# Performance work log

Hardware: AMD Instinct MI355X
Metric: run time of the kernel (lower is better)

## Reference

```python
import jax, jax.numpy as jnp
import numpy as np

EMBED = 768
DIM = 800          # embed + 32 gender features
IN_C = 1024
GRID = 32          # img_size // patch_size(=1)
LN_EPS = 1e-5      # torch nn.LayerNorm default


def setup_inputs() -> dict:
    key = jax.random.key(0)
    ks = jax.random.split(key, 8)
    B = 32
    x = jax.random.normal(ks[0], (B, IN_C, GRID, GRID), dtype=jnp.float32)
    gender_encode = jax.random.normal(ks[1], (B, 32), dtype=jnp.float32)
    # PatchEmbed 1x1 conv (acts as per-pixel linear) + LayerNorm params
    conv_w = jax.random.normal(ks[2], (EMBED, IN_C), dtype=jnp.float32) * (IN_C ** -0.5)
    conv_b = jnp.zeros((EMBED,), dtype=jnp.float32)
    ln_g = jnp.ones((EMBED,), dtype=jnp.float32)
    ln_b = jnp.zeros((EMBED,), dtype=jnp.float32)
    cls_token = jax.random.normal(ks[3], (1, 1, EMBED), dtype=jnp.float32) * 0.02
    # Attention qkv linear (bias=True); proj is never used in the forward path
    qkv_w = jax.random.normal(ks[4], (3 * DIM, DIM), dtype=jnp.float32) * (DIM ** -0.5)
    qkv_b = jnp.zeros((3 * DIM,), dtype=jnp.float32)
    return {
        "x": x, "gender_encode": gender_encode,
        "conv_w": conv_w, "conv_b": conv_b,
        "ln_g": ln_g, "ln_b": ln_b,
        "cls_token": cls_token,
        "qkv_w": qkv_w, "qkv_b": qkv_b,
    }


def _forward(x, gender_encode, conv_w, conv_b, ln_g, ln_b, cls_token, qkv_w, qkv_b):
    B = x.shape[0]
    # PatchEmbed: 1x1 conv stride 1 == per-pixel linear; flatten(2).transpose(1,2)
    p = jnp.einsum('bchw,oc->bhwo', x, conv_w) + conv_b        # [B,32,32,768]
    p = p.reshape(B, GRID * GRID, EMBED)                        # [B,1024,768]
    mu = jnp.mean(p, axis=-1, keepdims=True)
    var = jnp.mean((p - mu) ** 2, axis=-1, keepdims=True)
    p = (p - mu) * jax.lax.rsqrt(var + LN_EPS) * ln_g + ln_b
    # prepend cls token, concat broadcast gender features
    cls = jnp.broadcast_to(cls_token, (B, 1, EMBED))
    t = jnp.concatenate([cls, p], axis=1)                       # [B,1025,768]
    g = jnp.broadcast_to(gender_encode[:, None, :], (B, t.shape[1], 32))
    t = jnp.concatenate([t, g], axis=2)                         # [B,1025,800]
    # Attention (note: self.norm / proj / v are unused in the original forward)
    qkv = t @ qkv_w.T + qkv_b                                   # [B,1025,2400]
    q = qkv[..., 0:DIM]
    k = qkv[..., DIM:2 * DIM]
    scale = DIM ** -0.5
    # only the cls-query row is ever used -> compute just that row
    scores = jnp.einsum('bc,bnc->bn', q[:, 0], k) * scale       # [B,1025]
    attn_cls = jax.nn.softmax(scores[:, 1:], axis=-1)           # [B,1024]
    return attn_cls.reshape(B, 1, GRID, GRID)


def reference(x, gender_encode, conv_w, conv_b, ln_g, ln_b, cls_token, qkv_w, qkv_b):
    return _forward(x, gender_encode, conv_w, conv_b, ln_g, ln_b, cls_token, qkv_w, qkv_b)
```

## Files before the change

kernel.cpp:

```cpp
#include <hip/hip_runtime.h>
#include <hip/hip_bf16.h>

#define EMBED 768
#define DIMQ  800
#define INC   1024
#define NPIX  1024

typedef __bf16 bf16_t;
typedef __bf16 bf16x8 __attribute__((ext_vector_type(8)));
typedef __bf16 bf16x2 __attribute__((ext_vector_type(2)));
typedef float  f32x4  __attribute__((ext_vector_type(4)));

#define GLD_LDS(gp, lp) __builtin_amdgcn_global_load_lds( \
    (const __attribute__((address_space(1))) void*)(gp),  \
    (__attribute__((address_space(3))) void*)(lp), 16, 0, 0)

__global__ __launch_bounds__(256)
void k_prep(const float* __restrict__ x, bf16_t* __restrict__ xT,
            const float* __restrict__ w, bf16_t* __restrict__ cw,
            const float* __restrict__ qkv_w, const float* __restrict__ qkv_b,
            const float* __restrict__ cls, const float* __restrict__ gender,
            float* __restrict__ q0b) {
    __shared__ __align__(16) unsigned int tile[64 * 36];
    const int bi = blockIdx.x;
    const int t  = threadIdx.x;
    if (bi < 8192) {
        const int b  = bi >> 8;
        const int k0 = ((bi >> 4) & 15) * 64;
        const int m0 = (bi & 15) * 64;
        const int m_l = t & 63;
        const int wv  = t >> 6;
        const float* src = x + ((size_t)(b * 1024 + k0 + wv * 16) * 1024) + m0 + m_l;
        bf16x2* trow = (bf16x2*)tile;
#pragma unroll
        for (int i = 0; i < 8; ++i) {
            float a0 = src[(size_t)(2 * i) * 1024];
            float a1 = src[(size_t)(2 * i + 1) * 1024];
            bf16x2 p; p[0] = (bf16_t)a0; p[1] = (bf16_t)a1;
            trow[m_l * 36 + wv * 8 + i] = p;
        }
        __syncthreads();
        const int m_r = t >> 2;
        bf16_t* drow = xT + ((size_t)(b * 1024 + m0 + m_r) * 1024) + k0;
#pragma unroll
        for (int rep = 0; rep < 2; ++rep) {
            int j = (t & 3) + rep * 4;
            bf16x8 v = *(const bf16x8*)&tile[m_r * 36 + j * 4];
            int slot = j ^ (m_r & 7);
            *(bf16x8*)(drow + slot * 8) = v;
        }
    } else if (bi < 8392) {
        const int wv = t >> 6, tl = t & 63;
        const int i = (bi - 8192) * 4 + wv;
        const float* row = qkv_w + (size_t)i * DIMQ;
        float ps = 0.f;
        for (int j = tl; j < EMBED; j += 64) ps += row[j] * cls[j];
#pragma unroll
        for (int off = 1; off < 64; off <<= 1) ps += __shfl_xor(ps, off, 64);
        if (tl < 32) {
            float g = 0.f;
#pragma unroll
            for (int j = 0; j < 32; ++j) g += row[EMBED + j] * gender[tl * 32 + j];
            q0b[tl * DIMQ + i] = ps + g + qkv_b[i];
        }
    } else {
        const int i = (bi - 8392) * 256 + t;
        const int n = i >> 10, k = i & 1023;
        const int s = (k >> 3) & 7;
        const int src_k = (k & ~63) | (((s ^ (n & 7)) & 7) << 3) | (k & 7);
        cw[i] = (bf16_t)w[(size_t)n * 1024 + src_k];
    }
}

__global__ __launch_bounds__(256)
void k_u(const float* __restrict__ qkv_w, const float* __restrict__ q0b,
         const float* __restrict__ ln_g, float* __restrict__ u) {
    __shared__ float q0s[DIMQ];
    __shared__ float sh[8][33];
    int t = threadIdx.x;
    int b  = blockIdx.x / 24;
    int j0 = (blockIdx.x % 24) * 32;
    for (int i = t; i < DIMQ; i += 256) q0s[i] = q0b[b * DIMQ + i];
    __syncthreads();
    int j_l = t & 31, os = t >> 5;
    const float* wk = qkv_w + (size_t)DIMQ * DIMQ;
    const float* wp = wk + (size_t)(os * 100) * DIMQ + j0 + j_l;
    float acc = 0.f;
#pragma unroll 4
    for (int i = 0; i < 100; ++i) acc += wp[(size_t)i * DIMQ] * q0s[os * 100 + i];
    sh[os][j_l] = acc;
    __syncthreads();
    if (t < 32) {
        float s = 0.f;
#pragma unroll
        for (int o = 0; o < 8; ++o) s += sh[o][t];
        u[b * EMBED + j0 + t] = s * ln_g[j0 + t];
    }
}

__global__ __launch_bounds__(512, 2)
void k_main(const bf16_t* __restrict__ xT, const bf16_t* __restrict__ cw,
            const float* __restrict__ conv_b, const float* __restrict__ u,
            float* __restrict__ partial) {
    extern __shared__ unsigned char smem[];

    const int tid = threadIdx.x;
    const int bi = blockIdx.x;
    const int x8 = bi & 7;
    const int s  = bi >> 3;
    const int nt = s % 3;
    const int mt = (s / 3) * 8 + x8;
    const int b  = mt >> 2;
    const int gm = mt * 256;
    const int gn = nt * 256;

    const int wv = tid >> 6;
    const int l  = tid & 63;
    const int lr = l >> 3;
    const int lc = l & 7;

    const int col  = l & 15;
    const int quad = l >> 4;
    const int wm   = (wv >> 2) * 128;
    const int wn   = (wv & 3) * 64;

    bf16_t* A0 = (bf16_t*)(smem);
    bf16_t* B0 = (bf16_t*)(smem + 32768);
    bf16_t* A1 = (bf16_t*)(smem + 65536);
    bf16_t* B1 = (bf16_t*)(smem + 98304);

    const bf16_t* asrc = xT + (size_t)(gm + lr) * 1024 + lc * 8;
    const bf16_t* bsrc = cw + (size_t)(gn + lr) * 1024 + lc * 8;

    f32x4 C[8][4] = {};

#define ISSUE(tt, Ab, Bb) do {                                              \
        const size_t ko_ = (size_t)(tt) * 64;                               \
        _Pragma("unroll")                                                   \
        for (int j = 0; j < 4; ++j) {                                       \
            const int rg = j * 64 + wv * 8;                                 \
            GLD_LDS(asrc + (size_t)rg * 1024 + ko_, (Ab) + rg * 64);        \
            GLD_LDS(bsrc + (size_t)rg * 1024 + ko_, (Bb) + rg * 64);        \
        }                                                                   \
    } while (0)

    ISSUE(0, A0, B0);
    ISSUE(1, A1, B1);
    asm volatile("s_waitcnt vmcnt(8)" ::: "memory");
    asm volatile("s_barrier" ::: "memory");

    for (int t = 0; t < 16; ++t) {
        bf16_t* Ab = (t & 1) ? A1 : A0;
        bf16_t* Bb = (t & 1) ? B1 : B0;
#pragma unroll
        for (int ks = 0; ks < 2; ++ks) {
            bf16x8 bg[4];
#pragma unroll
            for (int ni = 0; ni < 4; ++ni) {
                const int r  = wn + ni * 16 + col;
                const int ph = (ks * 4 + quad) ^ (r & 7);
                bg[ni] = *(const bf16x8*)(Bb + r * 64 + ph * 8);
            }
#pragma unroll
            for (int g = 0; g < 2; ++g) {
                bf16x8 af[4];
#pragma unroll
                for (int mi = 0; mi < 4; ++mi) {
                    const int r  = wm + (g * 4 + mi) * 16 + col;
                    const int ph = (ks * 4 + quad) ^ (r & 7);
                    af[mi] = *(const bf16x8*)(Ab + r * 64 + ph * 8);
                }
                __builtin_amdgcn_s_barrier();
                __builtin_amdgcn_s_setprio(1);
#pragma unroll
                for (int mi = 0; mi < 4; ++mi)
#pragma unroll
                    for (int ni = 0; ni < 4; ++ni)
                        C[g * 4 + mi][ni] = __builtin_amdgcn_mfma_f32_16x16x32_bf16(
                            af[mi], bg[ni], C[g * 4 + mi][ni], 0, 0, 0);
                __builtin_amdgcn_s_setprio(0);
                __builtin_amdgcn_s_barrier();
            }
        }
        if (t < 15) {
            asm volatile("s_barrier" ::: "memory");
            if (t + 2 < 16) {
                bf16_t* An = (t & 1) ? A1 : A0;
                bf16_t* Bn = (t & 1) ? B1 : B0;
                ISSUE(t + 2, An, Bn);
                asm volatile("s_waitcnt vmcnt(8)" ::: "memory");
            } else {
                asm volatile("s_waitcnt vmcnt(0)" ::: "memory");
            }
            asm volatile("s_barrier" ::: "memory");
        }
    }
#undef ISSUE

    float cb[4], uv[4];
#pragma unroll
    for (int ni = 0; ni < 4; ++ni) {
        const int og = gn + wn + ni * 16 + col;
        cb[ni] = conv_b[og];
        uv[ni] = u[b * EMBED + og];
    }
    float* part = (float*)smem;
    asm volatile("s_barrier" ::: "memory");
#pragma unroll
    for (int mi = 0; mi < 8; ++mi)
#pragma unroll
        for (int r = 0; r < 4; ++r) {
            float a = 0.f, sq = 0.f, d = 0.f;
#pragma unroll
            for (int ni = 0; ni < 4; ++ni) {
                float v = C[mi][ni][r] + cb[ni];
                a += v; sq += v * v; d += v * uv[ni];
            }
#pragma unroll
            for (int off = 1; off < 16; off <<= 1) {
                a  += __shfl_xor(a, off, 64);
                sq += __shfl_xor(sq, off, 64);
                d  += __shfl_xor(d, off, 64);
            }
            if (col == 0) {
                const int row = wm + mi * 16 + quad * 4 + r;
                float* pp = part + ((wv & 3) * 256 + row) * 3;
                pp[0] = a; pp[1] = sq; pp[2] = d;
            }
        }
    __syncthreads();
    if (tid < 256) {
        float s1 = 0.f, s2 = 0.f, s3 = 0.f;
#pragma unroll
        for (int g2 = 0; g2 < 4; ++g2) {
            const float* pp = part + (g2 * 256 + tid) * 3;
            s1 += pp[0]; s2 += pp[1]; s3 += pp[2];
        }
        const size_t pix = (size_t)gm + tid;
        partial[(size_t)(0 * 3 + nt) * 32768 + pix] = s1;
        partial[(size_t)(1 * 3 + nt) * 32768 + pix] = s2;
        partial[(size_t)(2 * 3 + nt) * 32768 + pix] = s3;
    }
}

__global__ __launch_bounds__(1024)
void k_final(const float* __restrict__ partial, const float* __restrict__ u,
             float* __restrict__ out) {
    __shared__ float red[16];
    __shared__ float bc[3];
    const int b = blockIdx.x, t = threadIdx.x;
    const int lane = t & 63, wid = t >> 6;

    float pu = (t < EMBED) ? u[b * EMBED + t] : 0.f;
#pragma unroll
    for (int off = 1; off < 64; off <<= 1) pu += __shfl_xor(pu, off, 64);
    if (lane == 0) red[wid] = pu;
    __syncthreads();
    if (t == 0) { float s = 0.f; for (int i = 0; i < 16; ++i) s += red[i]; bc[0] = s; }
    __syncthreads();
    const float Su = bc[0];

    const size_t m = (size_t)b * 1024 + t;
    float S1 = 0.f, S2 = 0.f, S3 = 0.f;
#pragma unroll
    for (int nt = 0; nt < 3; ++nt) {
        S1 += partial[(size_t)(0 * 3 + nt) * 32768 + m];
        S2 += partial[(size_t)(1 * 3 + nt) * 32768 + m];
        S3 += partial[(size_t)(2 * 3 + nt) * 32768 + m];
    }
    const float mu  = S1 * (1.f / 768.f);
    const float var = S2 * (1.f / 768.f) - mu * mu;
    const float sc  = 0.035355339059327376f * (S3 - mu * Su) * rsqrtf(var + 1e-5f);

    float mx = sc;
#pragma unroll
    for (int off = 1; off < 64; off <<= 1) mx = fmaxf(mx, __shfl_xor(mx, off, 64));
    if (lane == 0) red[wid] = mx;
    __syncthreads();
    if (t == 0) { float mm = -1e30f; for (int i = 0; i < 16; ++i) mm = fmaxf(mm, red[i]); bc[1] = mm; }
    __syncthreads();
    const float e = __expf(sc - bc[1]);
    float ss = e;
#pragma unroll
    for (int off = 1; off < 64; off <<= 1) ss += __shfl_xor(ss, off, 64);
    __syncthreads();
    if (lane == 0) red[wid] = ss;
    __syncthreads();
    if (t == 0) { float s = 0.f; for (int i = 0; i < 16; ++i) s += red[i]; bc[2] = s; }
    __syncthreads();
    out[m] = e / bc[2];
}

extern "C" void kernel_launch(void* const* d_in, const int* in_sizes, int n_in,
                              void* d_out, int out_size, void* d_ws, size_t ws_size,
                              hipStream_t stream) {
    const float* x      = (const float*)d_in[0];
    const float* gender = (const float*)d_in[1];
    const float* conv_w = (const float*)d_in[2];
    const float* conv_b = (const float*)d_in[3];
    const float* ln_g   = (const float*)d_in[4];
    const float* cls    = (const float*)d_in[6];
    const float* qkv_w  = (const float*)d_in[7];
    const float* qkv_b  = (const float*)d_in[8];
    float* out = (float*)d_out;

    char* ws = (char*)d_ws;
    bf16_t* cw      = (bf16_t*)ws;
    float*  q0b     = (float*)(ws + 1572864);
    float*  u       = (float*)(ws + 1675264);
    float*  partial = (float*)(ws + 1773568);
    bf16_t* xT      = (bf16_t*)(ws + 4132864);

    static bool s_attr = false;
    if (!s_attr) {
        hipFuncSetAttribute(reinterpret_cast<const void*>(k_main),
                            hipFuncAttributeMaxDynamicSharedMemorySize, 131072);
        s_attr = true;
    }

    hipLaunchKernelGGL(k_prep,  dim3(11464), dim3(256),  0, stream,
                       x, xT, conv_w, cw, qkv_w, qkv_b, cls, gender, q0b);
    hipLaunchKernelGGL(k_u,     dim3(768),   dim3(256),  0, stream, qkv_w, q0b, ln_g, u);
    hipLaunchKernelGGL(k_main,  dim3(384),   dim3(512),  131072, stream, xT, cw, conv_b, u, partial);
    hipLaunchKernelGGL(k_final, dim3(32),    dim3(1024), 0, stream, partial, u, out);
}
```

Measured before the change: 322.4 us.

## Stream conv weights from global into registers and retile N to 192

The conv weight (B operand) is no longer staged in LDS. Each wave now loads its B fragments straight from global memory into registers, one k-step ahead, so the weight swizzle in the prep kernel is dropped. The N tile shrinks from 256 to 192, which gives 512 blocks instead of 384 and four partial slices per pixel instead of three. The A tile moves to a triple-buffered LDS ring using 96KB, with a simpler barrier and wait scheme. In exchange, B traffic goes through L2 directly with less reuse, and the implicit waits on the register loads may also serialize the A prefetch.

```diff
diff --git a/kernel.cpp b/kernel.cpp
--- a/kernel.cpp
+++ b/kernel.cpp
@@ -65,10 +65,7 @@
         }
     } else {
         const int i = (bi - 8392) * 256 + t;
-        const int n = i >> 10, k = i & 1023;
-        const int s = (k >> 3) & 7;
-        const int src_k = (k & ~63) | (((s ^ (n & 7)) & 7) << 3) | (k & 7);
-        cw[i] = (bf16_t)w[(size_t)n * 1024 + src_k];
+        cw[i] = (bf16_t)w[i];
     }
 }
 
@@ -108,11 +105,11 @@
     const int bi = blockIdx.x;
     const int x8 = bi & 7;
     const int s  = bi >> 3;
-    const int nt = s % 3;
-    const int mt = (s / 3) * 8 + x8;
+    const int nt = s & 3;
+    const int mt = (s >> 2) * 8 + x8;
     const int b  = mt >> 2;
     const int gm = mt * 256;
-    const int gn = nt * 256;
+    const int gn = nt * 192;
 
     const int wv = tid >> 6;
     const int l  = tid & 63;
@@ -122,45 +119,55 @@
     const int col  = l & 15;
     const int quad = l >> 4;
     const int wm   = (wv >> 2) * 128;
-    const int wn   = (wv & 3) * 64;
-
-    bf16_t* A0 = (bf16_t*)(smem);
-    bf16_t* B0 = (bf16_t*)(smem + 32768);
-    bf16_t* A1 = (bf16_t*)(smem + 65536);
-    bf16_t* B1 = (bf16_t*)(smem + 98304);
+    const int wn   = (wv & 3) * 48;
 
     const bf16_t* asrc = xT + (size_t)(gm + lr) * 1024 + lc * 8;
-    const bf16_t* bsrc = cw + (size_t)(gn + lr) * 1024 + lc * 8;
-
-    f32x4 C[8][4] = {};
-
-#define ISSUE(tt, Ab, Bb) do {                                              \
+    const bf16_t* bgp  = cw + (size_t)(gn + wn + col) * 1024 + quad * 8;
+
+    f32x4 C[8][3] = {};
+    bf16x8 bgC[2][3], bgN[2][3];
+
+#define ISSUE_A(tt, dst) do {                                               \
         const size_t ko_ = (size_t)(tt) * 64;                               \
         _Pragma("unroll")                                                   \
         for (int j = 0; j < 4; ++j) {                                       \
             const int rg = j * 64 + wv * 8;                                 \
-            GLD_LDS(asrc + (size_t)rg * 1024 + ko_, (Ab) + rg * 64);        \
-            GLD_LDS(bsrc + (size_t)rg * 1024 + ko_, (Bb) + rg * 64);        \
+            GLD_LDS(asrc + (size_t)rg * 1024 + ko_, (dst) + rg * 64);       \
         }                                                                   \
     } while (0)
 
-    ISSUE(0, A0, B0);
-    ISSUE(1, A1, B1);
-    asm volatile("s_waitcnt vmcnt(8)" ::: "memory");
-    asm volatile("s_barrier" ::: "memory");
-
+#define LOAD_BG(dst, tt) do {                                               \
+        _Pragma("unroll")                                                   \
+        for (int ks_ = 0; ks_ < 2; ++ks_)                                   \
+            _Pragma("unroll")                                               \
+            for (int ni_ = 0; ni_ < 3; ++ni_)                               \
+                dst[ks_][ni_] = *(const bf16x8*)(bgp + (size_t)(ni_ * 16) * 1024 \
+                                                 + (size_t)(tt) * 64 + ks_ * 32); \
+    } while (0)
+
+    ISSUE_A(0, (bf16_t*)(smem));
+    ISSUE_A(1, (bf16_t*)(smem + 32768));
+    __builtin_amdgcn_sched_barrier(0);
+    LOAD_BG(bgN, 0);
+    __builtin_amdgcn_sched_barrier(0);
+    asm volatile("s_waitcnt vmcnt(0)" ::: "memory");
+    __builtin_amdgcn_s_barrier();
+
+#pragma unroll 1
     for (int t = 0; t < 16; ++t) {
-        bf16_t* Ab = (t & 1) ? A1 : A0;
-        bf16_t* Bb = (t & 1) ? B1 : B0;
-#pragma unroll
-        for (int ks = 0; ks < 2; ++ks) {
-            bf16x8 bg[4];
-#pragma unroll
-            for (int ni = 0; ni < 4; ++ni) {
-                const int r  = wn + ni * 16 + col;
-                const int ph = (ks * 4 + quad) ^ (r & 7);
-                bg[ni] = *(const bf16x8*)(Bb + r * 64 + ph * 8);
-            }
+        bf16_t* Acur = (bf16_t*)(smem + (t % 3) * 32768);
+        __builtin_amdgcn_sched_barrier(0);
+        if (t + 2 < 16) ISSUE_A(t + 2, (bf16_t*)(smem + ((t + 2) % 3) * 32768));
+        __builtin_amdgcn_sched_barrier(0);
+#pragma unroll
+        for (int ks = 0; ks < 2; ++ks)
+#pragma unroll
+            for (int ni = 0; ni < 3; ++ni) bgC[ks][ni] = bgN[ks][ni];
+        if (t + 1 < 16) LOAD_BG(bgN, t + 1);
+        __builtin_amdgcn_sched_barrier(0);
+
+#pragma unroll
+        for (int ks = 0; ks < 2; ++ks)
 #pragma unroll
             for (int g = 0; g < 2; ++g) {
                 bf16x8 af[4];
@@ -168,51 +175,38 @@
                 for (int mi = 0; mi < 4; ++mi) {
                     const int r  = wm + (g * 4 + mi) * 16 + col;
                     const int ph = (ks * 4 + quad) ^ (r & 7);
-                    af[mi] = *(const bf16x8*)(Ab + r * 64 + ph * 8);
+                    af[mi] = *(const bf16x8*)(Acur + r * 64 + ph * 8);
                 }
                 __builtin_amdgcn_s_barrier();
                 __builtin_amdgcn_s_setprio(1);
 #pragma unroll
                 for (int mi = 0; mi < 4; ++mi)
 #pragma unroll
-                    for (int ni = 0; ni < 4; ++ni)
+                    for (int ni = 0; ni < 3; ++ni)
                         C[g * 4 + mi][ni] = __builtin_amdgcn_mfma_f32_16x16x32_bf16(
-                            af[mi], bg[ni], C[g * 4 + mi][ni], 0, 0, 0);
+                            af[mi], bgC[ks][ni], C[g * 4 + mi][ni], 0, 0, 0);
                 __builtin_amdgcn_s_setprio(0);
                 __builtin_amdgcn_s_barrier();
             }
-        }
-        if (t < 15) {
-            asm volatile("s_barrier" ::: "memory");
-            if (t + 2 < 16) {
-                bf16_t* An = (t & 1) ? A1 : A0;
-                bf16_t* Bn = (t & 1) ? B1 : B0;
-                ISSUE(t + 2, An, Bn);
-                asm volatile("s_waitcnt vmcnt(8)" ::: "memory");
-            } else {
-                asm volatile("s_waitcnt vmcnt(0)" ::: "memory");
-            }
-            asm volatile("s_barrier" ::: "memory");
-        }
-    }
-#undef ISSUE
-
-    float cb[4], uv[4];
-#pragma unroll
-    for (int ni = 0; ni < 4; ++ni) {
+    }
+#undef ISSUE_A
+#undef LOAD_BG
+
+    float cb[3], uv[3];
+#pragma unroll
+    for (int ni = 0; ni < 3; ++ni) {
         const int og = gn + wn + ni * 16 + col;
         cb[ni] = conv_b[og];
         uv[ni] = u[b * EMBED + og];
     }
     float* part = (float*)smem;
-    asm volatile("s_barrier" ::: "memory");
 #pragma unroll
     for (int mi = 0; mi < 8; ++mi)
 #pragma unroll
         for (int r = 0; r < 4; ++r) {
             float a = 0.f, sq = 0.f, d = 0.f;
 #pragma unroll
-            for (int ni = 0; ni < 4; ++ni) {
+            for (int ni = 0; ni < 3; ++ni) {
                 float v = C[mi][ni][r] + cb[ni];
                 a += v; sq += v * v; d += v * uv[ni];
             }
@@ -237,9 +231,9 @@
             s1 += pp[0]; s2 += pp[1]; s3 += pp[2];
         }
         const size_t pix = (size_t)gm + tid;
-        partial[(size_t)(0 * 3 + nt) * 32768 + pix] = s1;
-        partial[(size_t)(1 * 3 + nt) * 32768 + pix] = s2;
-        partial[(size_t)(2 * 3 + nt) * 32768 + pix] = s3;
+        partial[(size_t)(0 * 4 + nt) * 32768 + pix] = s1;
+        partial[(size_t)(1 * 4 + nt) * 32768 + pix] = s2;
+        partial[(size_t)(2 * 4 + nt) * 32768 + pix] = s3;
     }
 }
 
@@ -263,10 +257,10 @@
     const size_t m = (size_t)b * 1024 + t;
     float S1 = 0.f, S2 = 0.f, S3 = 0.f;
 #pragma unroll
-    for (int nt = 0; nt < 3; ++nt) {
-        S1 += partial[(size_t)(0 * 3 + nt) * 32768 + m];
-        S2 += partial[(size_t)(1 * 3 + nt) * 32768 + m];
-        S3 += partial[(size_t)(2 * 3 + nt) * 32768 + m];
+    for (int nt = 0; nt < 4; ++nt) {
+        S1 += partial[(size_t)(0 * 4 + nt) * 32768 + m];
+        S2 += partial[(size_t)(1 * 4 + nt) * 32768 + m];
+        S3 += partial[(size_t)(2 * 4 + nt) * 32768 + m];
     }
     const float mu  = S1 * (1.f / 768.f);
     const float var = S2 * (1.f / 768.f) - mu * mu;
@@ -314,13 +308,13 @@
     static bool s_attr = false;
     if (!s_attr) {
         hipFuncSetAttribute(reinterpret_cast<const void*>(k_main),
-                            hipFuncAttributeMaxDynamicSharedMemorySize, 131072);
+                            hipFuncAttributeMaxDynamicSharedMemorySize, 98304);
         s_attr = true;
     }
 
     hipLaunchKernelGGL(k_prep,  dim3(11464), dim3(256),  0, stream,
                        x, xT, conv_w, cw, qkv_w, qkv_b, cls, gender, q0b);
     hipLaunchKernelGGL(k_u,     dim3(768),   dim3(256),  0, stream, qkv_w, q0b, ln_g, u);
-    hipLaunchKernelGGL(k_main,  dim3(384),   dim3(512),  131072, stream, xT, cw, conv_b, u, partial);
+    hipLaunchKernelGGL(k_main,  dim3(512),   dim3(512),  98304, stream, xT, cw, conv_b, u, partial);
     hipLaunchKernelGGL(k_final, dim3(32),    dim3(1024), 0, stream, partial, u, out);
 }
```

After: 337.6 us. 1.05x slower.
